# Performance work log

Hardware: AMD Instinct MI355X
Metric: run time of the kernel (lower is better)

## Reference

```python
import jax, jax.numpy as jnp
from jax import lax
import numpy as np
import math

D_MODEL = 1024
D_STATE = 16
DT_RANK = 64  # ceil(1024/16)


def setup_inputs() -> dict:
    key = jax.random.key(0)
    ks = jax.random.split(key, 8)
    B, L = 2, 2048
    x = jax.random.normal(ks[0], (B, L, D_MODEL), dtype=jnp.float32)
    A_log = jnp.full((D_MODEL, D_STATE), math.log(0.5), dtype=jnp.float32)
    x_proj_w = jax.random.normal(ks[1], (DT_RANK + 2 * D_STATE, D_MODEL), dtype=jnp.float32) * (D_MODEL ** -0.5)
    dt_init_std = DT_RANK ** -0.5
    dt_proj_w = jax.random.uniform(ks[2], (D_MODEL, DT_RANK), minval=-dt_init_std, maxval=dt_init_std, dtype=jnp.float32)
    # dt bias init: softplus-inverse of dt sampled log-uniform in [2*dt_min, 2*dt_max] (trend)
    dt = jnp.exp(jax.random.uniform(ks[3], (D_MODEL,), dtype=jnp.float32) * (math.log(0.2) - math.log(0.002)) + math.log(0.002))
    dt = jnp.clip(dt, 1e-4)
    dt_proj_b = dt + jnp.log(-jnp.expm1(-dt))
    D_param = jnp.ones((D_MODEL,), dtype=jnp.float32)
    trend_emphasis = jnp.full((D_MODEL,), 0.1, dtype=jnp.float32)
    return {
        "x": x, "A_log": A_log, "x_proj_w": x_proj_w,
        "dt_proj_w": dt_proj_w, "dt_proj_b": dt_proj_b,
        "D_param": D_param, "trend_emphasis": trend_emphasis,
    }


def _selective_scan(u, delta, A, Bp, Cp, D_param):
    # u, delta: [B,L,D]; A: [D,N]; Bp, Cp: [B,L,N]; D_param: [D]
    deltaA = jnp.exp(jnp.einsum('bld,dn->bldn', delta, A))       # [B,L,D,N]
    deltaBu = jnp.einsum('bld,bln->bldn', delta * u, Bp)          # [B,L,D,N]
    Bsz, L, Dm, N = deltaA.shape

    def step(h, inp):
        dA, dBu, c = inp          # dA,dBu: [B,D,N]; c: [B,N]
        h = dA * h + dBu
        y = jnp.einsum('bdn,bn->bd', h, c)
        return h, y

    h0 = jnp.zeros((Bsz, Dm, N), dtype=u.dtype)
    xs = (jnp.moveaxis(deltaA, 1, 0), jnp.moveaxis(deltaBu, 1, 0), jnp.moveaxis(Cp, 1, 0))
    _, ys = lax.scan(step, h0, xs)            # ys: [L,B,D]
    y = jnp.moveaxis(ys, 0, 1)                # [B,L,D]
    return y + u * D_param


def reference(x, A_log, x_proj_w, dt_proj_w, dt_proj_b, D_param, trend_emphasis):
    # trend component: channel-wise emphasis gate (dropout in eval mode = identity)
    x = x * jax.nn.sigmoid(trend_emphasis)
    xz = x @ x_proj_w.T                                  # [B,L,dt_rank+2N]
    delta_part = xz[..., :DT_RANK]
    Bp = xz[..., DT_RANK:DT_RANK + D_STATE]              # [B,L,N]
    Cp = xz[..., DT_RANK + D_STATE:]                     # [B,L,N]
    delta = jax.nn.softplus(delta_part @ dt_proj_w.T + dt_proj_b)  # [B,L,D]
    A = -jnp.exp(A_log.astype(jnp.float32))
    return _selective_scan(x, delta, A, Bp, Cp, D_param.astype(jnp.float32))
```

## Files before the change

### kernel.cpp

```cpp
#include <hip/hip_runtime.h>
#include <math.h>


#define LOG2E 1.44269504088896340736f

__device__ __forceinline__ float fexp2(float v){
#if defined(__has_builtin)
#if __has_builtin(__builtin_amdgcn_exp2f)
  return __builtin_amdgcn_exp2f(v);
#else
  return exp2f(v);
#endif
#else
  return exp2f(v);
#endif
}

__global__ __launch_bounds__(256) void k_prep(const float* __restrict__ xpw,
                                              const float* __restrict__ dtw,
                                              const float* __restrict__ alog,
                                              const float* __restrict__ te,
                                              float* __restrict__ w2T,
                                              float* __restrict__ dtwT,
                                              float* __restrict__ A2,
                                              float* __restrict__ sg){
  __shared__ float sm[32 * 33];
  const int bid = blockIdx.x, t = threadIdx.x;
  const int lane = t & 31, srow = t >> 5;
  if (bid < 96){
    const int kt = bid / 3, ct = bid - kt * 3;
#pragma unroll
    for (int r = 0; r < 4; r++){
      const int cr = srow * 4 + r;
      sm[cr * 33 + lane] = xpw[(size_t)(ct * 32 + cr) * 1024 + kt * 32 + lane];
    }
    __syncthreads();
#pragma unroll
    for (int r = 0; r < 4; r++){
      const int kr = srow * 4 + r;
      const int kg = kt * 32 + kr;
      const float s = 1.f / (1.f + __expf(-te[kg]));
      w2T[(size_t)kg * 96 + ct * 32 + lane] = sm[lane * 33 + kr] * s;
    }
  } else if (bid < 160){
    const int idx = bid - 96, dti = idx >> 1, kt2 = idx & 1;
#pragma unroll
    for (int r = 0; r < 4; r++){
      const int cr = srow * 4 + r;
      sm[cr * 33 + lane] = dtw[(size_t)(dti * 32 + cr) * 64 + kt2 * 32 + lane];
    }
    __syncthreads();
#pragma unroll
    for (int r = 0; r < 4; r++){
      const int kr = srow * 4 + r;
      dtwT[(size_t)(kt2 * 32 + kr) * 1024 + dti * 32 + lane] = sm[lane * 33 + kr];
    }
  } else if (bid < 176){
    const int j = (bid - 160) * 1024 + t;
#pragma unroll
    for (int i = 0; i < 4; i++)
      A2[j + i * 256] = -__expf(alog[j + i * 256]) * LOG2E;
  } else {
#pragma unroll
    for (int i = 0; i < 4; i++){
      const int m = i * 256 + t;
      sg[m] = 1.f / (1.f + __expf(-te[m]));
    }
  }
}

__global__ __launch_bounds__(256) void k_xz(const float* __restrict__ x,
                                            const float* __restrict__ w2T,
                                            float* __restrict__ xzp){
  __shared__ float xT[32 * 257];
  const int t = threadIdx.x;
  const int row0 = blockIdx.x * 256;
  const int c0 = blockIdx.y * 32;
  const int kbase = blockIdx.z * 64;
  float acc[32];
#pragma unroll
  for (int c = 0; c < 32; c++) acc[c] = 0.f;
  const int kq = t & 7, rsub = t >> 3;
  for (int kt = 0; kt < 2; ++kt){
    const int k0 = kbase + kt * 32;
    __syncthreads();
#pragma unroll
    for (int p = 0; p < 8; p++){
      const int r = p * 32 + rsub;
      const float4 v = *reinterpret_cast<const float4*>(&x[(size_t)(row0 + r) * 1024 + k0 + kq * 4]);
      xT[(kq * 4 + 0) * 257 + r] = v.x;
      xT[(kq * 4 + 1) * 257 + r] = v.y;
      xT[(kq * 4 + 2) * 257 + r] = v.z;
      xT[(kq * 4 + 3) * 257 + r] = v.w;
    }
    __syncthreads();
#pragma unroll 4
    for (int kk = 0; kk < 32; ++kk){
      const float xv = xT[kk * 257 + t];
      const float* wr = &w2T[(size_t)(k0 + kk) * 96 + c0];
#pragma unroll
      for (int c = 0; c < 32; c++) acc[c] = fmaf(xv, wr[c], acc[c]);
    }
  }
  float4* o = reinterpret_cast<float4*>(xzp + ((size_t)blockIdx.z * 4096 + row0 + t) * 96 + c0);
  const float4* av = reinterpret_cast<const float4*>(acc);
#pragma unroll
  for (int q = 0; q < 8; q++) o[q] = av[q];
}

__global__ __launch_bounds__(256) void k_reduce(const float4* __restrict__ p,
                                                float4* __restrict__ xz){
  const int i = blockIdx.x * 256 + threadIdx.x;
  float4 r = p[i];
#pragma unroll
  for (int s = 1; s < 16; s++){
    const float4 a = p[(size_t)s * 98304 + i];
    r.x += a.x; r.y += a.y; r.z += a.z; r.w += a.w;
  }
  xz[i] = r;
}

__global__ __launch_bounds__(256) void k_scan1(const float* __restrict__ x,
                                               const float* __restrict__ xz,
                                               const float* __restrict__ dtwT,
                                               const float* __restrict__ dtb,
                                               const float* __restrict__ A2,
                                               const float* __restrict__ sg,
                                               float* __restrict__ S,
                                               float* __restrict__ P){
  const int t = threadIdx.x;
  const int chunk = blockIdx.x, dgrp = blockIdx.y, b = blockIdx.z;
  const int d = dgrp * 256 + t;
  const int l0 = chunk * 32;
  float w[64];
#pragma unroll
  for (int k = 0; k < 64; k++) w[k] = dtwT[(size_t)k * 1024 + d];
  float a2[16];
  {
    const float4* ap = reinterpret_cast<const float4*>(A2 + (size_t)d * 16);
#pragma unroll
    for (int q = 0; q < 4; q++){
      const float4 v = ap[q];
      a2[q*4] = v.x; a2[q*4+1] = v.y; a2[q*4+2] = v.z; a2[q*4+3] = v.w;
    }
  }
  bool uni = true;
#pragma unroll
  for (int n = 1; n < 16; n++) uni = uni && (a2[n] == a2[0]);
  const float sgv = sg[d], dtbv = dtb[d];
  const float* xzb = xz + (size_t)(b * 2048 + l0) * 96;
  float dl[32];
#pragma unroll 4
  for (int li = 0; li < 32; ++li){
    float a = dtbv;
    const float* dp = xzb + li * 96;
#pragma unroll
    for (int k = 0; k < 64; k++) a = fmaf(dp[k], w[k], a);
    dl[li] = fmaxf(a, 0.f) + log1pf(__expf(-fabsf(a)));
  }
  float h[16];
#pragma unroll
  for (int n = 0; n < 16; n++) h[n] = 0.f;
  const size_t xidx = (size_t)(b * 2048 + l0) * 1024 + d;
  const size_t base = ((size_t)((b * 64 + chunk) * 1024 + d)) * 16;
  if (uni){
    const float a2u = a2[0];
    float Ppu = 1.f;
#pragma unroll 4
    for (int li = 0; li < 32; ++li){
      const float dv = dl[li];
      const float xv = x[xidx + (size_t)li * 1024];
      const float du = dv * xv * sgv;
      const float tt = fexp2(dv * a2u);
      Ppu *= tt;
      const float* brow = xzb + li * 96 + 64;
#pragma unroll
      for (int n = 0; n < 16; n++) h[n] = fmaf(tt, h[n], du * brow[n]);
    }
#pragma unroll
    for (int q = 0; q < 4; q++){
      float4 v; v.x = h[q*4]; v.y = h[q*4+1]; v.z = h[q*4+2]; v.w = h[q*4+3];
      *reinterpret_cast<float4*>(&S[base + q * 4]) = v;
      float4 u; u.x = Ppu; u.y = Ppu; u.z = Ppu; u.w = Ppu;
      *reinterpret_cast<float4*>(&P[base + q * 4]) = u;
    }
  } else {
    float Pp[16];
#pragma unroll
    for (int n = 0; n < 16; n++) Pp[n] = 1.f;
    for (int li = 0; li < 32; ++li){
      const float dv = dl[li];
      const float xv = x[xidx + (size_t)li * 1024];
      const float du = dv * xv * sgv;
      const float* brow = xzb + li * 96 + 64;
#pragma unroll
      for (int n = 0; n < 16; n++){
        const float tt = fexp2(dv * a2[n]);
        h[n] = fmaf(tt, h[n], du * brow[n]);
        Pp[n] *= tt;
      }
    }
#pragma unroll
    for (int q = 0; q < 4; q++){
      float4 v; v.x = h[q*4]; v.y = h[q*4+1]; v.z = h[q*4+2]; v.w = h[q*4+3];
      *reinterpret_cast<float4*>(&S[base + q * 4]) = v;
      float4 u; u.x = Pp[q*4]; u.y = Pp[q*4+1]; u.z = Pp[q*4+2]; u.w = Pp[q*4+3];
      *reinterpret_cast<float4*>(&P[base + q * 4]) = u;
    }
  }
}

__global__ __launch_bounds__(128) void k_scan2(const float* __restrict__ S,
                                               const float* __restrict__ P,
                                               float* __restrict__ H){
  const int g = blockIdx.x * 128 + threadIdx.x;
  const int n = g & 15, dd = (g >> 4) & 1023, bb = g >> 14;
  float h = 0.f;
#pragma unroll 8
  for (int c = 0; c < 64; c++){
    const size_t idx = ((size_t)((bb * 64 + c) * 1024 + dd)) * 16 + n;
    H[idx] = h;
    h = fmaf(P[idx], h, S[idx]);
  }
}

__global__ __launch_bounds__(256) void k_scan3(const float* __restrict__ x,
                                               const float* __restrict__ xz,
                                               const float* __restrict__ dtwT,
                                               const float* __restrict__ dtb,
                                               const float* __restrict__ A2,
                                               const float* __restrict__ sg,
                                               const float* __restrict__ Dpar,
                                               const float* __restrict__ H,
                                               float* __restrict__ out){
  const int t = threadIdx.x;
  const int chunk = blockIdx.x, dgrp = blockIdx.y, b = blockIdx.z;
  const int d = dgrp * 256 + t;
  const int l0 = chunk * 32;
  float w[64];
#pragma unroll
  for (int k = 0; k < 64; k++) w[k] = dtwT[(size_t)k * 1024 + d];
  float a2[16];
  {
    const float4* ap = reinterpret_cast<const float4*>(A2 + (size_t)d * 16);
#pragma unroll
    for (int q = 0; q < 4; q++){
      const float4 v = ap[q];
      a2[q*4] = v.x; a2[q*4+1] = v.y; a2[q*4+2] = v.z; a2[q*4+3] = v.w;
    }
  }
  bool uni = true;
#pragma unroll
  for (int n = 1; n < 16; n++) uni = uni && (a2[n] == a2[0]);
  const float sgv = sg[d], dtbv = dtb[d], Dv = Dpar[d];
  const float* xzb = xz + (size_t)(b * 2048 + l0) * 96;
  float dl[32];
#pragma unroll 4
  for (int li = 0; li < 32; ++li){
    float a = dtbv;
    const float* dp = xzb + li * 96;
#pragma unroll
    for (int k = 0; k < 64; k++) a = fmaf(dp[k], w[k], a);
    dl[li] = fmaxf(a, 0.f) + log1pf(__expf(-fabsf(a)));
  }
  float h[16];
  {
    const float4* hp = reinterpret_cast<const float4*>(H + ((size_t)((b * 64 + chunk) * 1024 + d)) * 16);
#pragma unroll
    for (int q = 0; q < 4; q++){
      const float4 v = hp[q];
      h[q*4] = v.x; h[q*4+1] = v.y; h[q*4+2] = v.z; h[q*4+3] = v.w;
    }
  }
  const size_t xidx = (size_t)(b * 2048 + l0) * 1024 + d;
  if (uni){
    const float a2u = a2[0];
#pragma unroll 4
    for (int li = 0; li < 32; ++li){
      const float dv = dl[li];
      const float xv = x[xidx + (size_t)li * 1024];
      const float du = dv * xv * sgv;
      const float tt = fexp2(dv * a2u);
      const float* brow = xzb + li * 96 + 64;
      float y = 0.f;
#pragma unroll
      for (int n = 0; n < 16; n++){
        h[n] = fmaf(tt, h[n], du * brow[n]);
        y = fmaf(h[n], brow[16 + n], y);
      }
      out[xidx + (size_t)li * 1024] = fmaf(xv * sgv, Dv, y);
    }
  } else {
    for (int li = 0; li < 32; ++li){
      const float dv = dl[li];
      const float xv = x[xidx + (size_t)li * 1024];
      const float du = dv * xv * sgv;
      const float* brow = xzb + li * 96 + 64;
      float y = 0.f;
#pragma unroll
      for (int n = 0; n < 16; n++){
        const float tt = fexp2(dv * a2[n]);
        h[n] = fmaf(tt, h[n], du * brow[n]);
        y = fmaf(h[n], brow[16 + n], y);
      }
      out[xidx + (size_t)li * 1024] = fmaf(xv * sgv, Dv, y);
    }
  }
}

extern "C" void kernel_launch(void* const* d_in, const int* in_sizes, int n_in,
                              void* d_out, int out_size, void* d_ws, size_t ws_size,
                              hipStream_t stream){
  const float* x    = (const float*)d_in[0];
  const float* Alog = (const float*)d_in[1];
  const float* xpw  = (const float*)d_in[2];
  const float* dtw  = (const float*)d_in[3];
  const float* dtb  = (const float*)d_in[4];
  const float* Dpar = (const float*)d_in[5];
  const float* te   = (const float*)d_in[6];
  float* out = (float*)d_out;
  char* ws = (char*)d_ws;

  float* w2T  = (float*)(ws);
  float* A2   = (float*)(ws + 393216);
  float* sg   = (float*)(ws + 458752);
  float* dtwT = (float*)(ws + 462848);
  float* xz   = (float*)(ws + 724992);
  float* xzp  = (float*)(ws + 2297856);
  float* S    = (float*)(ws + 27463680);
  float* P    = (float*)(ws + 35852288);
  float* Hst  = (float*)(ws + 44240896);

  hipLaunchKernelGGL(k_prep,   dim3(177),        dim3(256), 0, stream, xpw, dtw, Alog, te, w2T, dtwT, A2, sg);
  hipLaunchKernelGGL(k_xz,     dim3(16, 3, 16),  dim3(256), 0, stream, x, w2T, xzp);
  hipLaunchKernelGGL(k_reduce, dim3(384),        dim3(256), 0, stream, (const float4*)xzp, (float4*)xz);
  hipLaunchKernelGGL(k_scan1,  dim3(64, 4, 2),   dim3(256), 0, stream, x, xz, dtwT, dtb, A2, sg, S, P);
  hipLaunchKernelGGL(k_scan2,  dim3(256),        dim3(128), 0, stream, S, P, Hst);
  hipLaunchKernelGGL(k_scan3,  dim3(64, 4, 2),   dim3(256), 0, stream, x, xz, dtwT, dtb, A2, sg, Dpar, Hst, out);
}
```

Before: 184.5 us.

## Halve scan chunk length, use packed float2 math, and compute decay product from summed delta

The scan chunk size drops from 32 to 16, which doubles the number of chunks and blocks in scan1 and scan3. This is meant to expose more parallelism, at the price of larger S/P/H buffers and a longer serial loop in scan2. The xz GEMM, the delta projection and the state updates are rewritten with 2-wide float vectors so the compiler can emit packed FMA instructions. The uniform-A decay product is now computed with a single exp2 of the summed delta instead of a running product, and softplus switches to fast __logf.

```diff
diff --git a/kernel.cpp b/kernel.cpp
--- a/kernel.cpp
+++ b/kernel.cpp
@@ -3,6 +3,7 @@
 
 
 #define LOG2E 1.44269504088896340736f
+typedef float v2f __attribute__((ext_vector_type(2)));
 
 __device__ __forceinline__ float fexp2(float v){
 #if defined(__has_builtin)
@@ -14,6 +15,10 @@
 #else
   return exp2f(v);
 #endif
+}
+
+__device__ __forceinline__ float fsoftplus(float v){
+  return fmaxf(v, 0.f) + __logf(1.f + __expf(-fabsf(v)));
 }
 
 __global__ __launch_bounds__(256) void k_prep(const float* __restrict__ xpw,
@@ -77,9 +82,9 @@
   const int row0 = blockIdx.x * 256;
   const int c0 = blockIdx.y * 32;
   const int kbase = blockIdx.z * 64;
-  float acc[32];
-#pragma unroll
-  for (int c = 0; c < 32; c++) acc[c] = 0.f;
+  v2f acc[16];
+#pragma unroll
+  for (int c = 0; c < 16; c++) acc[c] = (v2f){0.f, 0.f};
   const int kq = t & 7, rsub = t >> 3;
   for (int kt = 0; kt < 2; ++kt){
     const int k0 = kbase + kt * 32;
@@ -97,9 +102,10 @@
 #pragma unroll 4
     for (int kk = 0; kk < 32; ++kk){
       const float xv = xT[kk * 257 + t];
-      const float* wr = &w2T[(size_t)(k0 + kk) * 96 + c0];
-#pragma unroll
-      for (int c = 0; c < 32; c++) acc[c] = fmaf(xv, wr[c], acc[c]);
+      const v2f xv2 = {xv, xv};
+      const v2f* wr = reinterpret_cast<const v2f*>(&w2T[(size_t)(k0 + kk) * 96 + c0]);
+#pragma unroll
+      for (int c = 0; c < 16; c++) acc[c] = acc[c] + xv2 * wr[c];
     }
   }
   float4* o = reinterpret_cast<float4*>(xzp + ((size_t)blockIdx.z * 4096 + row0 + t) * 96 + c0);
@@ -131,10 +137,13 @@
   const int t = threadIdx.x;
   const int chunk = blockIdx.x, dgrp = blockIdx.y, b = blockIdx.z;
   const int d = dgrp * 256 + t;
-  const int l0 = chunk * 32;
-  float w[64];
-#pragma unroll
-  for (int k = 0; k < 64; k++) w[k] = dtwT[(size_t)k * 1024 + d];
+  const int l0 = chunk * 16;
+  v2f wv[32];
+#pragma unroll
+  for (int k2 = 0; k2 < 32; k2++){
+    wv[k2].x = dtwT[(size_t)(2 * k2) * 1024 + d];
+    wv[k2].y = dtwT[(size_t)(2 * k2 + 1) * 1024 + d];
+  }
   float a2[16];
   {
     const float4* ap = reinterpret_cast<const float4*>(A2 + (size_t)d * 16);
@@ -149,46 +158,49 @@
   for (int n = 1; n < 16; n++) uni = uni && (a2[n] == a2[0]);
   const float sgv = sg[d], dtbv = dtb[d];
   const float* xzb = xz + (size_t)(b * 2048 + l0) * 96;
-  float dl[32];
-#pragma unroll 4
-  for (int li = 0; li < 32; ++li){
-    float a = dtbv;
-    const float* dp = xzb + li * 96;
-#pragma unroll
-    for (int k = 0; k < 64; k++) a = fmaf(dp[k], w[k], a);
-    dl[li] = fmaxf(a, 0.f) + log1pf(__expf(-fabsf(a)));
-  }
-  float h[16];
-#pragma unroll
-  for (int n = 0; n < 16; n++) h[n] = 0.f;
+  float dl[16];
+#pragma unroll
+  for (int li = 0; li < 16; ++li){
+    v2f acc = {dtbv, 0.f};
+    const v2f* dp = reinterpret_cast<const v2f*>(xzb + li * 96);
+#pragma unroll
+    for (int k2 = 0; k2 < 32; k2++) acc = acc + dp[k2] * wv[k2];
+    dl[li] = fsoftplus(acc.x + acc.y);
+  }
   const size_t xidx = (size_t)(b * 2048 + l0) * 1024 + d;
-  const size_t base = ((size_t)((b * 64 + chunk) * 1024 + d)) * 16;
+  const size_t base = ((size_t)((b * 128 + chunk) * 1024 + d)) * 16;
   if (uni){
     const float a2u = a2[0];
-    float Ppu = 1.f;
+    v2f h2[8];
+#pragma unroll
+    for (int q = 0; q < 8; q++) h2[q] = (v2f){0.f, 0.f};
+    float sumd = 0.f;
 #pragma unroll 4
-    for (int li = 0; li < 32; ++li){
+    for (int li = 0; li < 16; ++li){
       const float dv = dl[li];
+      sumd += dv;
       const float xv = x[xidx + (size_t)li * 1024];
       const float du = dv * xv * sgv;
       const float tt = fexp2(dv * a2u);
-      Ppu *= tt;
-      const float* brow = xzb + li * 96 + 64;
-#pragma unroll
-      for (int n = 0; n < 16; n++) h[n] = fmaf(tt, h[n], du * brow[n]);
-    }
-#pragma unroll
-    for (int q = 0; q < 4; q++){
-      float4 v; v.x = h[q*4]; v.y = h[q*4+1]; v.z = h[q*4+2]; v.w = h[q*4+3];
-      *reinterpret_cast<float4*>(&S[base + q * 4]) = v;
-      float4 u; u.x = Ppu; u.y = Ppu; u.z = Ppu; u.w = Ppu;
-      *reinterpret_cast<float4*>(&P[base + q * 4]) = u;
-    }
+      const v2f tt2 = {tt, tt}, du2 = {du, du};
+      const v2f* brow = reinterpret_cast<const v2f*>(xzb + li * 96 + 64);
+#pragma unroll
+      for (int q = 0; q < 8; q++) h2[q] = h2[q] * tt2 + brow[q] * du2;
+    }
+    const float Ppu = fexp2(a2u * sumd);
+    const float4* hv = reinterpret_cast<const float4*>(h2);
+#pragma unroll
+    for (int q = 0; q < 4; q++)
+      *reinterpret_cast<float4*>(&S[base + q * 4]) = hv[q];
+    const float4 pv = {Ppu, Ppu, Ppu, Ppu};
+#pragma unroll
+    for (int q = 0; q < 4; q++)
+      *reinterpret_cast<float4*>(&P[base + q * 4]) = pv;
   } else {
-    float Pp[16];
-#pragma unroll
-    for (int n = 0; n < 16; n++) Pp[n] = 1.f;
-    for (int li = 0; li < 32; ++li){
+    float h[16], Pp[16];
+#pragma unroll
+    for (int n = 0; n < 16; n++){ h[n] = 0.f; Pp[n] = 1.f; }
+    for (int li = 0; li < 16; ++li){
       const float dv = dl[li];
       const float xv = x[xidx + (size_t)li * 1024];
       const float du = dv * xv * sgv;
@@ -217,8 +229,8 @@
   const int n = g & 15, dd = (g >> 4) & 1023, bb = g >> 14;
   float h = 0.f;
 #pragma unroll 8
-  for (int c = 0; c < 64; c++){
-    const size_t idx = ((size_t)((bb * 64 + c) * 1024 + dd)) * 16 + n;
+  for (int c = 0; c < 128; c++){
+    const size_t idx = ((size_t)((bb * 128 + c) * 1024 + dd)) * 16 + n;
     H[idx] = h;
     h = fmaf(P[idx], h, S[idx]);
   }
@@ -236,10 +248,13 @@
   const int t = threadIdx.x;
   const int chunk = blockIdx.x, dgrp = blockIdx.y, b = blockIdx.z;
   const int d = dgrp * 256 + t;
-  const int l0 = chunk * 32;
-  float w[64];
-#pragma unroll
-  for (int k = 0; k < 64; k++) w[k] = dtwT[(size_t)k * 1024 + d];
+  const int l0 = chunk * 16;
+  v2f wv[32];
+#pragma unroll
+  for (int k2 = 0; k2 < 32; k2++){
+    wv[k2].x = dtwT[(size_t)(2 * k2) * 1024 + d];
+    wv[k2].y = dtwT[(size_t)(2 * k2 + 1) * 1024 + d];
+  }
   float a2[16];
   {
     const float4* ap = reinterpret_cast<const float4*>(A2 + (size_t)d * 16);
@@ -254,44 +269,54 @@
   for (int n = 1; n < 16; n++) uni = uni && (a2[n] == a2[0]);
   const float sgv = sg[d], dtbv = dtb[d], Dv = Dpar[d];
   const float* xzb = xz + (size_t)(b * 2048 + l0) * 96;
-  float dl[32];
-#pragma unroll 4
-  for (int li = 0; li < 32; ++li){
-    float a = dtbv;
-    const float* dp = xzb + li * 96;
-#pragma unroll
-    for (int k = 0; k < 64; k++) a = fmaf(dp[k], w[k], a);
-    dl[li] = fmaxf(a, 0.f) + log1pf(__expf(-fabsf(a)));
-  }
-  float h[16];
-  {
-    const float4* hp = reinterpret_cast<const float4*>(H + ((size_t)((b * 64 + chunk) * 1024 + d)) * 16);
-#pragma unroll
-    for (int q = 0; q < 4; q++){
-      const float4 v = hp[q];
-      h[q*4] = v.x; h[q*4+1] = v.y; h[q*4+2] = v.z; h[q*4+3] = v.w;
-    }
+  float dl[16];
+#pragma unroll
+  for (int li = 0; li < 16; ++li){
+    v2f acc = {dtbv, 0.f};
+    const v2f* dp = reinterpret_cast<const v2f*>(xzb + li * 96);
+#pragma unroll
+    for (int k2 = 0; k2 < 32; k2++) acc = acc + dp[k2] * wv[k2];
+    dl[li] = fsoftplus(acc.x + acc.y);
   }
   const size_t xidx = (size_t)(b * 2048 + l0) * 1024 + d;
+  const size_t hbase = ((size_t)((b * 128 + chunk) * 1024 + d)) * 16;
   if (uni){
     const float a2u = a2[0];
+    v2f h2[8];
+    {
+      const float4* hp = reinterpret_cast<const float4*>(H + hbase);
+      float4* hd = reinterpret_cast<float4*>(h2);
+#pragma unroll
+      for (int q = 0; q < 4; q++) hd[q] = hp[q];
+    }
 #pragma unroll 4
-    for (int li = 0; li < 32; ++li){
+    for (int li = 0; li < 16; ++li){
       const float dv = dl[li];
       const float xv = x[xidx + (size_t)li * 1024];
       const float du = dv * xv * sgv;
       const float tt = fexp2(dv * a2u);
-      const float* brow = xzb + li * 96 + 64;
-      float y = 0.f;
-#pragma unroll
-      for (int n = 0; n < 16; n++){
-        h[n] = fmaf(tt, h[n], du * brow[n]);
-        y = fmaf(h[n], brow[16 + n], y);
+      const v2f tt2 = {tt, tt}, du2 = {du, du};
+      const v2f* brow = reinterpret_cast<const v2f*>(xzb + li * 96 + 64);
+      const v2f* crow = reinterpret_cast<const v2f*>(xzb + li * 96 + 80);
+      v2f yv = {0.f, 0.f};
+#pragma unroll
+      for (int q = 0; q < 8; q++){
+        h2[q] = h2[q] * tt2 + brow[q] * du2;
+        yv = yv + h2[q] * crow[q];
       }
-      out[xidx + (size_t)li * 1024] = fmaf(xv * sgv, Dv, y);
+      out[xidx + (size_t)li * 1024] = fmaf(xv * sgv, Dv, yv.x + yv.y);
     }
   } else {
-    for (int li = 0; li < 32; ++li){
+    float h[16];
+    {
+      const float4* hp = reinterpret_cast<const float4*>(H + hbase);
+#pragma unroll
+      for (int q = 0; q < 4; q++){
+        const float4 v = hp[q];
+        h[q*4] = v.x; h[q*4+1] = v.y; h[q*4+2] = v.z; h[q*4+3] = v.w;
+      }
+    }
+    for (int li = 0; li < 16; ++li){
       const float dv = dl[li];
       const float xv = x[xidx + (size_t)li * 1024];
       const float du = dv * xv * sgv;
@@ -328,13 +353,13 @@
   float* xz   = (float*)(ws + 724992);
   float* xzp  = (float*)(ws + 2297856);
   float* S    = (float*)(ws + 27463680);
-  float* P    = (float*)(ws + 35852288);
-  float* Hst  = (float*)(ws + 44240896);
+  float* P    = (float*)(ws + 44240896);
+  float* Hst  = (float*)(ws + 61018112);
 
   hipLaunchKernelGGL(k_prep,   dim3(177),        dim3(256), 0, stream, xpw, dtw, Alog, te, w2T, dtwT, A2, sg);
   hipLaunchKernelGGL(k_xz,     dim3(16, 3, 16),  dim3(256), 0, stream, x, w2T, xzp);
   hipLaunchKernelGGL(k_reduce, dim3(384),        dim3(256), 0, stream, (const float4*)xzp, (float4*)xz);
-  hipLaunchKernelGGL(k_scan1,  dim3(64, 4, 2),   dim3(256), 0, stream, x, xz, dtwT, dtb, A2, sg, S, P);
+  hipLaunchKernelGGL(k_scan1,  dim3(128, 4, 2),  dim3(256), 0, stream, x, xz, dtwT, dtb, A2, sg, S, P);
   hipLaunchKernelGGL(k_scan2,  dim3(256),        dim3(128), 0, stream, S, P, Hst);
-  hipLaunchKernelGGL(k_scan3,  dim3(64, 4, 2),   dim3(256), 0, stream, x, xz, dtwT, dtb, A2, sg, Dpar, Hst, out);
-}
+  hipLaunchKernelGGL(k_scan3,  dim3(128, 4, 2),  dim3(256), 0, stream, x, xz, dtwT, dtb, A2, sg, Dpar, Hst, out);
+}
```

Result: faster. 163.7 us (-11.2%).
